# Kernel tuning notes

Hardware: AMD Instinct MI355X
Metric: run time of the kernel (lower is better)

## Reference

```python
import jax, jax.numpy as jnp
import numpy as np

D_MODEL = 1024   # 'seq_len' arg = input feature dim
FF_DIM = 1024
SCALE = 0.03125  # 1/sqrt(1024)


def setup_inputs() -> dict:
    key = jax.random.key(0)
    ks = jax.random.split(key, 7)
    B, T = 8, 2048
    s = 1.0 / np.sqrt(D_MODEL)
    return {
        "sequence": jax.random.normal(ks[0], (B, T, D_MODEL), dtype=jnp.float32),
        "Wq": jax.random.uniform(ks[1], (FF_DIM, D_MODEL), jnp.float32, -s, s),
        "bq": jax.random.uniform(ks[2], (FF_DIM,), jnp.float32, -s, s),
        "Wk": jax.random.uniform(ks[3], (FF_DIM, D_MODEL), jnp.float32, -s, s),
        "bk": jax.random.uniform(ks[4], (FF_DIM,), jnp.float32, -s, s),
        "Wv": jax.random.uniform(ks[5], (FF_DIM, D_MODEL), jnp.float32, -s, s),
        "bv": jax.random.uniform(ks[6], (FF_DIM,), jnp.float32, -s, s),
    }


def reference(sequence, Wq, bq, Wk, bk, Wv, bv):
    # Q/K/V linear projections (torch Linear: x @ W.T + b)
    q = jnp.einsum('btd,fd->btf', sequence, Wq) + bq
    k = jnp.einsum('btd,fd->btf', sequence, Wk) + bk
    v = jnp.einsum('btd,fd->btf', sequence, Wv) + bv
    # scaled dot-product attention (dropout p=0 -> identity)
    scores = jnp.einsum('btf,bsf->bts', q, k) * SCALE  # [B,T,T]
    attn = jax.nn.softmax(scores, axis=-1)
    return jnp.einsum('bts,bsf->btf', attn, v)
```

## Files before the change

### kernel.cpp

```cpp
#include <hip/hip_runtime.h>
#include <hip/hip_bf16.h>

#define BB 8
#define TT 2048
#define DD 1024
#define FF 1024

typedef __attribute__((ext_vector_type(8))) short bf16x8;
typedef __attribute__((ext_vector_type(4))) float f32x4;
typedef __attribute__((ext_vector_type(4))) short s16x4;

constexpr float kScaleLog2e = 0.03125f * 1.44269504088896340736f;

__device__ __forceinline__ short bf16_bits(float x) {
    __hip_bfloat16 h = __float2bfloat16(x);
    short s;
    __builtin_memcpy(&s, &h, sizeof(short));
    return s;
}

__global__ __launch_bounds__(256) void cvt_all(
    const float* __restrict__ seq, const float* __restrict__ Wq,
    const float* __restrict__ Wk, const float* __restrict__ Wv,
    short* __restrict__ seqb, short* __restrict__ Wb)
{
    const int bid = blockIdx.x;
    const float* src;
    short* dst;
    int i;
    if (bid < 8192)      { src = seq; dst = seqb;                      i = bid * 256 + threadIdx.x; }
    else if (bid < 8704) { src = Wq;  dst = Wb;                        i = (bid - 8192) * 256 + threadIdx.x; }
    else if (bid < 9216) { src = Wk;  dst = Wb + (size_t)FF * DD;      i = (bid - 8704) * 256 + threadIdx.x; }
    else                 { src = Wv;  dst = Wb + (size_t)2 * FF * DD;  i = (bid - 9216) * 256 + threadIdx.x; }
    f32x4 a = ((const f32x4*)src)[2 * i];
    f32x4 b = ((const f32x4*)src)[2 * i + 1];
    bf16x8 o;
#pragma unroll
    for (int j = 0; j < 4; ++j) { o[j] = bf16_bits(a[j]); o[4 + j] = bf16_bits(b[j]); }
    ((bf16x8*)dst)[i] = o;
}

#define SLOT 8192

__device__ __forceinline__ void stage2(const short* g0, const short* g1,
                                       short* slot, int lo0, int lo1) {
    __builtin_amdgcn_global_load_lds(
        (const __attribute__((address_space(1))) unsigned int*)g0,
        (__attribute__((address_space(3))) unsigned int*)(slot + lo0), 16, 0, 0);
    __builtin_amdgcn_global_load_lds(
        (const __attribute__((address_space(1))) unsigned int*)g1,
        (__attribute__((address_space(3))) unsigned int*)(slot + lo1), 16, 0, 0);
}

template<int W>
__device__ __forceinline__ void tile_barrier() {
    if constexpr (W == 8)      asm volatile("s_waitcnt vmcnt(8)" ::: "memory");
    else if constexpr (W == 4) asm volatile("s_waitcnt vmcnt(4)" ::: "memory");
    else if constexpr (W == 0) asm volatile("s_waitcnt vmcnt(0)" ::: "memory");
    __builtin_amdgcn_s_barrier();
    __builtin_amdgcn_sched_barrier(0);
}

__device__ __forceinline__ void lgkm_gate() {
    asm volatile("s_waitcnt lgkmcnt(0)" ::: "memory");
    __builtin_amdgcn_sched_barrier(0);
}

template<bool S12, bool S34, int WMID, int WEND>
__device__ __forceinline__ void tile_body(
    int t, short* As, short* Bs,
    const short* a0, const short* a1, const short* b0, const short* b1,
    int lo0, int lo1, int wm, int wn, int rk, f32x4 (&acc)[8][4])
{
    const short* sA0 = As + ((2 * t) & 3) * SLOT;
    const short* sB0 = Bs + ((2 * t) & 3) * SLOT;
    const short* sA1 = As + ((2 * t + 1) & 3) * SLOT;
    const short* sB1 = Bs + ((2 * t + 1) & 3) * SLOT;

    bf16x8 a[4], b[4];

#pragma unroll
    for (int m = 0; m < 4; ++m) a[m] = *(const bf16x8*)(sA0 + (wm + m * 16) * 32 + rk);
#pragma unroll
    for (int n = 0; n < 4; ++n) b[n] = *(const bf16x8*)(sB0 + (wn + n * 16) * 32 + rk);
    if constexpr (S12)
        stage2(a0 + (2 * t + 3) * 32, a1 + (2 * t + 3) * 32,
               As + ((2 * t + 3) & 3) * SLOT, lo0, lo1);
    lgkm_gate();
    __builtin_amdgcn_s_setprio(1);
#pragma unroll
    for (int m = 0; m < 4; ++m)
#pragma unroll
        for (int n = 0; n < 4; ++n)
            acc[m][n] = __builtin_amdgcn_mfma_f32_16x16x32_bf16(a[m], b[n], acc[m][n], 0, 0, 0);
    __builtin_amdgcn_s_setprio(0);

#pragma unroll
    for (int m = 0; m < 4; ++m) a[m] = *(const bf16x8*)(sA0 + (wm + 64 + m * 16) * 32 + rk);
    if constexpr (S12)
        stage2(b0 + (2 * t + 3) * 32, b1 + (2 * t + 3) * 32,
               Bs + ((2 * t + 3) & 3) * SLOT, lo0, lo1);
    lgkm_gate();
    __builtin_amdgcn_s_setprio(1);
#pragma unroll
    for (int m = 0; m < 4; ++m)
#pragma unroll
        for (int n = 0; n < 4; ++n)
            acc[m + 4][n] = __builtin_amdgcn_mfma_f32_16x16x32_bf16(a[m], b[n], acc[m + 4][n], 0, 0, 0);
    __builtin_amdgcn_s_setprio(0);

    tile_barrier<WMID>();

#pragma unroll
    for (int m = 0; m < 4; ++m) a[m] = *(const bf16x8*)(sA1 + (wm + m * 16) * 32 + rk);
#pragma unroll
    for (int n = 0; n < 4; ++n) b[n] = *(const bf16x8*)(sB1 + (wn + n * 16) * 32 + rk);
    if constexpr (S34)
        stage2(a0 + (2 * t + 4) * 32, a1 + (2 * t + 4) * 32,
               As + ((2 * t + 4) & 3) * SLOT, lo0, lo1);
    lgkm_gate();
    __builtin_amdgcn_s_setprio(1);
#pragma unroll
    for (int m = 0; m < 4; ++m)
#pragma unroll
        for (int n = 0; n < 4; ++n)
            acc[m][n] = __builtin_amdgcn_mfma_f32_16x16x32_bf16(a[m], b[n], acc[m][n], 0, 0, 0);
    __builtin_amdgcn_s_setprio(0);

#pragma unroll
    for (int m = 0; m < 4; ++m) a[m] = *(const bf16x8*)(sA1 + (wm + 64 + m * 16) * 32 + rk);
    if constexpr (S34)
        stage2(b0 + (2 * t + 4) * 32, b1 + (2 * t + 4) * 32,
               Bs + ((2 * t + 4) & 3) * SLOT, lo0, lo1);
    lgkm_gate();
    __builtin_amdgcn_s_setprio(1);
#pragma unroll
    for (int m = 0; m < 4; ++m)
#pragma unroll
        for (int n = 0; n < 4; ++n)
            acc[m + 4][n] = __builtin_amdgcn_mfma_f32_16x16x32_bf16(a[m], b[n], acc[m + 4][n], 0, 0, 0);
    __builtin_amdgcn_s_setprio(0);

    if constexpr (WEND >= 0)
        tile_barrier<WEND>();
}

__device__ __forceinline__ void gemm256(
    const short* __restrict__ A, int lda, int m0,
    const short* __restrict__ B, int ldb, int n0,
    int T, short* As, short* Bs, f32x4 (&acc)[8][4])
{
    const int tid  = threadIdx.x;
    const int lane = tid & 63;
    const int w    = tid >> 6;
    const int wm   = (w >> 2) * 128;
    const int wn   = (w & 3) * 64;
    const int r    = lane & 15;
    const int qd   = lane >> 4;
    const int rk   = r * 32 + (qd ^ ((r >> 1) & 3)) * 8;

    const int s0   = w * 128 + lane, s1 = s0 + 64;
    const int row0 = s0 >> 2,  row1 = s1 >> 2;
    const int cl0  = (s0 & 3) ^ ((row0 >> 1) & 3);
    const int cl1  = (s1 & 3) ^ ((row1 >> 1) & 3);
    const short* a0 = A + (size_t)(m0 + row0) * lda + cl0 * 8;
    const short* a1 = A + (size_t)(m0 + row1) * lda + cl1 * 8;
    const short* b0 = B + (size_t)(n0 + row0) * ldb + cl0 * 8;
    const short* b1 = B + (size_t)(n0 + row1) * ldb + cl1 * 8;
    const int lo0 = s0 * 8, lo1 = s1 * 8;

    stage2(a0,      a1,      As,            lo0, lo1);
    stage2(b0,      b1,      Bs,            lo0, lo1);
    stage2(a0 + 32, a1 + 32, As + SLOT,     lo0, lo1);
    stage2(b0 + 32, b1 + 32, Bs + SLOT,     lo0, lo1);
    stage2(a0 + 64, a1 + 64, As + 2 * SLOT, lo0, lo1);
    stage2(b0 + 64, b1 + 64, Bs + 2 * SLOT, lo0, lo1);
    tile_barrier<8>();

    for (int t = 0; t < T - 2; ++t)
        tile_body<true, true, 8, 8>(t, As, Bs, a0, a1, b0, b1, lo0, lo1, wm, wn, rk, acc);
    tile_body<true,  false, 8, 4>(T - 2, As, Bs, a0, a1, b0, b1, lo0, lo1, wm, wn, rk, acc);
    tile_body<false, false, 0, -1>(T - 1, As, Bs, a0, a1, b0, b1, lo0, lo1, wm, wn, rk, acc);
}

__global__ __launch_bounds__(512, 2) void qkv256(
    const short* __restrict__ seqb, const short* __restrict__ Wb,
    const float* __restrict__ bq, const float* __restrict__ bk,
    const float* __restrict__ bv,
    __hip_bfloat16* __restrict__ q, __hip_bfloat16* __restrict__ k,
    __hip_bfloat16* __restrict__ vT)
{
    __shared__ short As[4 * SLOT], Bs[4 * SLOT];
    const int bid  = blockIdx.x;
    const int id2  = (bid & 7) * 96 + (bid >> 3);
    const int mt   = id2 / 12;
    const int rest = id2 - mt * 12;
    const int nt   = rest & 3;
    const int proj = rest >> 2;

    const short* W    = Wb + (size_t)proj * FF * DD;
    const float* bias = proj == 0 ? bq : (proj == 1 ? bk : bv);

    f32x4 acc[8][4];
#pragma unroll
    for (int m = 0; m < 8; ++m)
#pragma unroll
        for (int n = 0; n < 4; ++n) acc[m][n] = (f32x4){0.f, 0.f, 0.f, 0.f};

    gemm256(seqb, DD, mt * 256, W, DD, nt * 256, DD / 64, As, Bs, acc);

    const int lane = threadIdx.x & 63;
    const int w    = threadIdx.x >> 6;
    const int wm   = (w >> 2) * 128;
    const int wn   = (w & 3) * 64;
    const int r    = lane & 15;
    const int qd   = lane >> 4;
    const int row_base = mt * 256 + wm + qd * 4;
    const int col_base = nt * 256 + wn + r;

    if (proj < 2) {
        __hip_bfloat16* dst = (proj == 0) ? q : k;
#pragma unroll
        for (int nf = 0; nf < 4; ++nf) {
            const int col = col_base + nf * 16;
            const float bv_ = bias[col];
#pragma unroll
            for (int mf = 0; mf < 8; ++mf)
#pragma unroll
                for (int i = 0; i < 4; ++i)
                    dst[(size_t)(row_base + mf * 16 + i) * FF + col] =
                        __float2bfloat16(acc[mf][nf][i] + bv_);
        }
    } else {
#pragma unroll
        for (int mf = 0; mf < 8; ++mf) {
            const int rowg = row_base + mf * 16;
            const int b_   = rowg >> 11;
            const int t_   = rowg & 2047;
            __hip_bfloat16* vb = vT + (size_t)b_ * FF * TT;
#pragma unroll
            for (int nf = 0; nf < 4; ++nf) {
                const int col = col_base + nf * 16;
                const float bvv = bias[col];
                s16x4 pack;
#pragma unroll
                for (int i = 0; i < 4; ++i) pack[i] = bf16_bits(acc[mf][nf][i] + bvv);
                *(s16x4*)(vb + (size_t)col * TT + t_) = pack;
            }
        }
    }
}

__global__ __launch_bounds__(512, 2) void score256(
    const __hip_bfloat16* __restrict__ q, const __hip_bfloat16* __restrict__ k,
    __hip_bfloat16* __restrict__ P, float* __restrict__ Z)
{
    __shared__ short As[4 * SLOT], Bs[4 * SLOT];
    const int bid = blockIdx.x;
    const int id2 = (bid & 7) * 64 + (bid >> 3);
    const int b   = id2 >> 6;
    const int tt  = (id2 >> 3) & 7;
    const int st  = id2 & 7;

    const short* qb = (const short*)q + (size_t)b * TT * FF;
    const short* kb = (const short*)k + (size_t)b * TT * FF;

    f32x4 acc[8][4];
#pragma unroll
    for (int m = 0; m < 8; ++m)
#pragma unroll
        for (int n = 0; n < 4; ++n) acc[m][n] = (f32x4){0.f, 0.f, 0.f, 0.f};

    gemm256(qb, FF, tt * 256, kb, FF, st * 256, FF / 64, As, Bs, acc);

    const int lane = threadIdx.x & 63;
    const int w    = threadIdx.x >> 6;
    const int wm   = (w >> 2) * 128;
    const int wn   = (w & 3) * 64;
    const int r    = lane & 15;
    const int qd   = lane >> 4;
    const int row_base = tt * 256 + wm + qd * 4;
    const int col_base = st * 256 + wn + r;

    __hip_bfloat16* Pb = P + (size_t)b * TT * TT;
    float* Zb = Z + b * TT;

    float rs[8][4];
#pragma unroll
    for (int mf = 0; mf < 8; ++mf)
#pragma unroll
        for (int i = 0; i < 4; ++i) rs[mf][i] = 0.f;

#pragma unroll
    for (int mf = 0; mf < 8; ++mf)
#pragma unroll
        for (int nf = 0; nf < 4; ++nf) {
            const int col = col_base + nf * 16;
#pragma unroll
            for (int i = 0; i < 4; ++i) {
                const float e = exp2f(acc[mf][nf][i] * kScaleLog2e);
                const __hip_bfloat16 eb = __float2bfloat16(e);
                rs[mf][i] += __bfloat162float(eb);
                Pb[(size_t)(row_base + mf * 16 + i) * TT + col] = eb;
            }
        }
#pragma unroll
    for (int off = 1; off < 16; off <<= 1)
#pragma unroll
        for (int mf = 0; mf < 8; ++mf)
#pragma unroll
            for (int i = 0; i < 4; ++i) rs[mf][i] += __shfl_xor(rs[mf][i], off, 64);
    if (r == 0) {
#pragma unroll
        for (int mf = 0; mf < 8; ++mf)
#pragma unroll
            for (int i = 0; i < 4; ++i)
                atomicAdd(&Zb[row_base + mf * 16 + i], rs[mf][i]);
    }
}

__global__ __launch_bounds__(512, 2) void pv256(
    const __hip_bfloat16* __restrict__ P, const __hip_bfloat16* __restrict__ vT,
    const float* __restrict__ Z, float* __restrict__ out)
{
    __shared__ short As[4 * SLOT], Bs[4 * SLOT];
    const int bid = blockIdx.x;
    const int id2 = (bid & 7) * 32 + (bid >> 3);
    const int b   = id2 >> 5;
    const int tt  = (id2 >> 2) & 7;
    const int ft  = id2 & 3;

    const short* Pb = (const short*)P + (size_t)b * TT * TT;
    const short* vb = (const short*)vT + (size_t)b * FF * TT;

    f32x4 acc[8][4];
#pragma unroll
    for (int m = 0; m < 8; ++m)
#pragma unroll
        for (int n = 0; n < 4; ++n) acc[m][n] = (f32x4){0.f, 0.f, 0.f, 0.f};

    gemm256(Pb, TT, tt * 256, vb, TT, ft * 256, TT / 64, As, Bs, acc);

    const int lane = threadIdx.x & 63;
    const int w    = threadIdx.x >> 6;
    const int wm   = (w >> 2) * 128;
    const int wn   = (w & 3) * 64;
    const int r    = lane & 15;
    const int qd   = lane >> 4;
    const int row_base = tt * 256 + wm + qd * 4;
    const int col_base = ft * 256 + wn + r;

    const float* Zb = Z + b * TT;
    float* ob = out + (size_t)b * TT * FF;

#pragma unroll
    for (int mf = 0; mf < 8; ++mf) {
        float rz[4];
#pragma unroll
        for (int i = 0; i < 4; ++i) rz[i] = 1.0f / Zb[row_base + mf * 16 + i];
#pragma unroll
        for (int nf = 0; nf < 4; ++nf) {
            const int col = col_base + nf * 16;
#pragma unroll
            for (int i = 0; i < 4; ++i)
                ob[(size_t)(row_base + mf * 16 + i) * FF + col] = acc[mf][nf][i] * rz[i];
        }
    }
}

extern "C" void kernel_launch(void* const* d_in, const int* in_sizes, int n_in,
                              void* d_out, int out_size, void* d_ws, size_t ws_size,
                              hipStream_t stream) {
    const float* seq = (const float*)d_in[0];
    const float* Wq  = (const float*)d_in[1];
    const float* bq  = (const float*)d_in[2];
    const float* Wk  = (const float*)d_in[3];
    const float* bk  = (const float*)d_in[4];
    const float* Wv  = (const float*)d_in[5];
    const float* bv  = (const float*)d_in[6];
    float* out = (float*)d_out;
    char* ws = (char*)d_ws;

    const size_t MB32 = 33554432;
    __hip_bfloat16* q   = (__hip_bfloat16*)(ws);
    __hip_bfloat16* k   = (__hip_bfloat16*)(ws + MB32);
    __hip_bfloat16* vT  = (__hip_bfloat16*)(ws + 2 * MB32);
    __hip_bfloat16* P   = (__hip_bfloat16*)(ws + 3 * MB32);
    float*          Z   = (float*)(ws + 3 * MB32 + (size_t)67108864);
    short*          seqb = (short*)P;
    short*          Wb   = (short*)((char*)P + MB32);

    hipMemsetAsync(Z, 0, (size_t)BB * TT * sizeof(float), stream);

    cvt_all<<<9728, 256, 0, stream>>>(seq, Wq, Wk, Wv, seqb, Wb);
    qkv256<<<768, 512, 0, stream>>>(seqb, Wb, bq, bk, bv, q, k, vT);
    score256<<<BB * 64, 512, 0, stream>>>(q, k, P, Z);
    pv256<<<BB * 32, 512, 0, stream>>>(P, vT, Z, out);
}
```

Baseline: 408.4 us.

## Software-pipeline LDS fragment loads ahead of MFMAs in QKV GEMM main loop

Restructures the QKV projection GEMM inner loop so LDS fragment reads for the next sub-tile are issued before the current MFMA block runs, and the first fragments of the next tile are prefetched into registers carried across iterations. Full lgkmcnt(0) gates are replaced by partial lgkmcnt waits, and there is now one vmcnt barrier per half-tile instead of two per tile. The aim is to hide LDS latency behind MFMA work, at the cost of more live registers (extra fragment arrays), which risks spills under launch_bounds(512,2).

```diff
diff --git a/kernel.cpp b/kernel.cpp
--- a/kernel.cpp
+++ b/kernel.cpp
@@ -52,97 +52,102 @@
         (__attribute__((address_space(3))) unsigned int*)(slot + lo1), 16, 0, 0);
 }
 
-template<int W>
-__device__ __forceinline__ void tile_barrier() {
-    if constexpr (W == 8)      asm volatile("s_waitcnt vmcnt(8)" ::: "memory");
-    else if constexpr (W == 4) asm volatile("s_waitcnt vmcnt(4)" ::: "memory");
-    else if constexpr (W == 0) asm volatile("s_waitcnt vmcnt(0)" ::: "memory");
-    __builtin_amdgcn_s_barrier();
-    __builtin_amdgcn_sched_barrier(0);
-}
-
-__device__ __forceinline__ void lgkm_gate() {
-    asm volatile("s_waitcnt lgkmcnt(0)" ::: "memory");
-    __builtin_amdgcn_sched_barrier(0);
-}
-
-template<bool S12, bool S34, int WMID, int WEND>
+__device__ __forceinline__ void sbar() { __builtin_amdgcn_sched_barrier(0); }
+
+template<int N>
+__device__ __forceinline__ void lgkm() {
+    if constexpr (N == 12)     asm volatile("s_waitcnt lgkmcnt(12)" ::: "memory");
+    else if constexpr (N == 8) asm volatile("s_waitcnt lgkmcnt(8)"  ::: "memory");
+    else if constexpr (N == 4) asm volatile("s_waitcnt lgkmcnt(4)"  ::: "memory");
+    else                       asm volatile("s_waitcnt lgkmcnt(0)"  ::: "memory");
+}
+
+__device__ __forceinline__ void mfma16(const bf16x8 (&a)[4], const bf16x8 (&b)[4],
+                                       f32x4 (&acc)[8][4], int mo) {
+#pragma unroll
+    for (int m = 0; m < 4; ++m)
+#pragma unroll
+        for (int n = 0; n < 4; ++n)
+            acc[m + mo][n] = __builtin_amdgcn_mfma_f32_16x16x32_bf16(a[m], b[n], acc[m + mo][n], 0, 0, 0);
+}
+
+template<int MODE>
 __device__ __forceinline__ void tile_body(
     int t, short* As, short* Bs,
-    const short* a0, const short* a1, const short* b0, const short* b1,
-    int lo0, int lo1, int wm, int wn, int rk, f32x4 (&acc)[8][4])
+    const short* a0g, const short* a1g, const short* b0g, const short* b1g,
+    int lo0, int lo1, int wm, int wn, int rk,
+    f32x4 (&acc)[8][4], bf16x8 (&ra)[4], bf16x8 (&rb)[4])
 {
     const short* sA0 = As + ((2 * t) & 3) * SLOT;
-    const short* sB0 = Bs + ((2 * t) & 3) * SLOT;
     const short* sA1 = As + ((2 * t + 1) & 3) * SLOT;
     const short* sB1 = Bs + ((2 * t + 1) & 3) * SLOT;
 
-    bf16x8 a[4], b[4];
-
-#pragma unroll
-    for (int m = 0; m < 4; ++m) a[m] = *(const bf16x8*)(sA0 + (wm + m * 16) * 32 + rk);
-#pragma unroll
-    for (int n = 0; n < 4; ++n) b[n] = *(const bf16x8*)(sB0 + (wn + n * 16) * 32 + rk);
-    if constexpr (S12)
-        stage2(a0 + (2 * t + 3) * 32, a1 + (2 * t + 3) * 32,
+    bf16x8 a2[4], a3[4], b3[4], a4[4];
+
+#pragma unroll
+    for (int m = 0; m < 4; ++m) a2[m] = *(const bf16x8*)(sA0 + (wm + 64 + m * 16) * 32 + rk);
+#pragma unroll
+    for (int m = 0; m < 4; ++m) a3[m] = *(const bf16x8*)(sA1 + (wm + m * 16) * 32 + rk);
+#pragma unroll
+    for (int n = 0; n < 4; ++n) b3[n] = *(const bf16x8*)(sB1 + (wn + n * 16) * 32 + rk);
+    if constexpr (MODE <= 1) {
+        stage2(a0g + (2 * t + 3) * 32, a1g + (2 * t + 3) * 32,
                As + ((2 * t + 3) & 3) * SLOT, lo0, lo1);
-    lgkm_gate();
+        stage2(b0g + (2 * t + 3) * 32, b1g + (2 * t + 3) * 32,
+               Bs + ((2 * t + 3) & 3) * SLOT, lo0, lo1);
+    }
+    sbar(); lgkm<12>(); sbar();
     __builtin_amdgcn_s_setprio(1);
-#pragma unroll
-    for (int m = 0; m < 4; ++m)
-#pragma unroll
-        for (int n = 0; n < 4; ++n)
-            acc[m][n] = __builtin_amdgcn_mfma_f32_16x16x32_bf16(a[m], b[n], acc[m][n], 0, 0, 0);
+    mfma16(ra, rb, acc, 0);
     __builtin_amdgcn_s_setprio(0);
 
 #pragma unroll
-    for (int m = 0; m < 4; ++m) a[m] = *(const bf16x8*)(sA0 + (wm + 64 + m * 16) * 32 + rk);
-    if constexpr (S12)
-        stage2(b0 + (2 * t + 3) * 32, b1 + (2 * t + 3) * 32,
-               Bs + ((2 * t + 3) & 3) * SLOT, lo0, lo1);
-    lgkm_gate();
+    for (int m = 0; m < 4; ++m) a4[m] = *(const bf16x8*)(sA1 + (wm + 64 + m * 16) * 32 + rk);
+    sbar(); lgkm<12>(); sbar();
     __builtin_amdgcn_s_setprio(1);
-#pragma unroll
-    for (int m = 0; m < 4; ++m)
-#pragma unroll
-        for (int n = 0; n < 4; ++n)
-            acc[m + 4][n] = __builtin_amdgcn_mfma_f32_16x16x32_bf16(a[m], b[n], acc[m + 4][n], 0, 0, 0);
+    mfma16(a2, rb, acc, 4);
     __builtin_amdgcn_s_setprio(0);
 
-    tile_barrier<WMID>();
-
-#pragma unroll
-    for (int m = 0; m < 4; ++m) a[m] = *(const bf16x8*)(sA1 + (wm + m * 16) * 32 + rk);
-#pragma unroll
-    for (int n = 0; n < 4; ++n) b[n] = *(const bf16x8*)(sB1 + (wn + n * 16) * 32 + rk);
-    if constexpr (S34)
-        stage2(a0 + (2 * t + 4) * 32, a1 + (2 * t + 4) * 32,
+    if constexpr (MODE <= 1) {
+        asm volatile("s_waitcnt vmcnt(4)" ::: "memory");
+        __builtin_amdgcn_s_barrier();
+        sbar();
+    }
+    if constexpr (MODE == 0) {
+        stage2(a0g + (2 * t + 4) * 32, a1g + (2 * t + 4) * 32,
                As + ((2 * t + 4) & 3) * SLOT, lo0, lo1);
-    lgkm_gate();
+        stage2(b0g + (2 * t + 4) * 32, b1g + (2 * t + 4) * 32,
+               Bs + ((2 * t + 4) & 3) * SLOT, lo0, lo1);
+    }
+    sbar(); lgkm<4>(); sbar();
     __builtin_amdgcn_s_setprio(1);
-#pragma unroll
-    for (int m = 0; m < 4; ++m)
-#pragma unroll
-        for (int n = 0; n < 4; ++n)
-            acc[m][n] = __builtin_amdgcn_mfma_f32_16x16x32_bf16(a[m], b[n], acc[m][n], 0, 0, 0);
+    mfma16(a3, b3, acc, 0);
     __builtin_amdgcn_s_setprio(0);
 
-#pragma unroll
-    for (int m = 0; m < 4; ++m) a[m] = *(const bf16x8*)(sA1 + (wm + 64 + m * 16) * 32 + rk);
-    if constexpr (S34)
-        stage2(b0 + (2 * t + 4) * 32, b1 + (2 * t + 4) * 32,
-               Bs + ((2 * t + 4) & 3) * SLOT, lo0, lo1);
-    lgkm_gate();
+    if constexpr (MODE <= 1) {
+        const short* sAn = As + ((2 * t + 2) & 3) * SLOT;
+        const short* sBn = Bs + ((2 * t + 2) & 3) * SLOT;
+#pragma unroll
+        for (int m = 0; m < 4; ++m) ra[m] = *(const bf16x8*)(sAn + (wm + m * 16) * 32 + rk);
+#pragma unroll
+        for (int n = 0; n < 4; ++n) rb[n] = *(const bf16x8*)(sBn + (wn + n * 16) * 32 + rk);
+    }
+    sbar();
+    if constexpr (MODE <= 1) { lgkm<8>(); } else { lgkm<0>(); }
+    sbar();
     __builtin_amdgcn_s_setprio(1);
-#pragma unroll
-    for (int m = 0; m < 4; ++m)
-#pragma unroll
-        for (int n = 0; n < 4; ++n)
-            acc[m + 4][n] = __builtin_amdgcn_mfma_f32_16x16x32_bf16(a[m], b[n], acc[m + 4][n], 0, 0, 0);
+    mfma16(a4, b3, acc, 4);
     __builtin_amdgcn_s_setprio(0);
 
-    if constexpr (WEND >= 0)
-        tile_barrier<WEND>();
+    if constexpr (MODE == 0) {
+        asm volatile("s_waitcnt vmcnt(4)" ::: "memory");
+        __builtin_amdgcn_s_barrier();
+        sbar();
+    } else if constexpr (MODE == 1) {
+        asm volatile("s_waitcnt vmcnt(0)" ::: "memory");
+        __builtin_amdgcn_s_barrier();
+        sbar();
+    }
 }
 
 __device__ __forceinline__ void gemm256(
@@ -175,12 +180,20 @@
     stage2(b0 + 32, b1 + 32, Bs + SLOT,     lo0, lo1);
     stage2(a0 + 64, a1 + 64, As + 2 * SLOT, lo0, lo1);
     stage2(b0 + 64, b1 + 64, Bs + 2 * SLOT, lo0, lo1);
-    tile_barrier<8>();
+    asm volatile("s_waitcnt vmcnt(4)" ::: "memory");
+    __builtin_amdgcn_s_barrier();
+    sbar();
+
+    bf16x8 ra[4], rb[4];
+#pragma unroll
+    for (int m = 0; m < 4; ++m) ra[m] = *(const bf16x8*)(As + (wm + m * 16) * 32 + rk);
+#pragma unroll
+    for (int n = 0; n < 4; ++n) rb[n] = *(const bf16x8*)(Bs + (wn + n * 16) * 32 + rk);
 
     for (int t = 0; t < T - 2; ++t)
-        tile_body<true, true, 8, 8>(t, As, Bs, a0, a1, b0, b1, lo0, lo1, wm, wn, rk, acc);
-    tile_body<true,  false, 8, 4>(T - 2, As, Bs, a0, a1, b0, b1, lo0, lo1, wm, wn, rk, acc);
-    tile_body<false, false, 0, -1>(T - 1, As, Bs, a0, a1, b0, b1, lo0, lo1, wm, wn, rk, acc);
+        tile_body<0>(t, As, Bs, a0, a1, b0, b1, lo0, lo1, wm, wn, rk, acc, ra, rb);
+    tile_body<1>(T - 2, As, Bs, a0, a1, b0, b1, lo0, lo1, wm, wn, rk, acc, ra, rb);
+    tile_body<2>(T - 1, As, Bs, a0, a1, b0, b1, lo0, lo1, wm, wn, rk, acc, ra, rb);
 }
 
 __global__ __launch_bounds__(512, 2) void qkv256(
```

New measurement: 410.8 us. About the same (+0.6%).

## Fold Wq and Wk into a combined matrix to drop the K projection

Applied to the files above, without the earlier changes.

Rewrites the scores as X·(Wq^T Wk)·X^T plus a per-key bias term, with terms that are constant along each softmax row dropped. A small GEMM forms W2 = Wq^T·Wk once per call and projects X with it in place of computing Q and K separately. The score GEMM then reads the bf16 X directly as keys. This removes one of the three large projection GEMMs and the K write, at the cost of a split-K weight GEMM, a reduction kernel, an extra bf16 rounding of the combined weights, and the key bias folded into the conversion pass via a dot product.

```diff
diff --git a/kernel.cpp b/kernel.cpp
--- a/kernel.cpp
+++ b/kernel.cpp
@@ -19,25 +19,92 @@
     return s;
 }
 
+__global__ __launch_bounds__(256) void wv2k(
+    const float* __restrict__ Wk, const float* __restrict__ bq,
+    float* __restrict__ wv2)
+{
+    const int d = blockIdx.x * 256 + threadIdx.x;
+    float acc = 0.f;
+#pragma unroll 8
+    for (int f = 0; f < 1024; ++f) acc += Wk[(size_t)f * 1024 + d] * bq[f];
+    wv2[d] = acc;
+}
+
 __global__ __launch_bounds__(256) void cvt_all(
     const float* __restrict__ seq, const float* __restrict__ Wq,
     const float* __restrict__ Wk, const float* __restrict__ Wv,
-    short* __restrict__ seqb, short* __restrict__ Wb)
-{
+    const float* __restrict__ wv2,
+    short* __restrict__ Xbuf, short* __restrict__ Wvb,
+    short* __restrict__ WqT, short* __restrict__ WkT,
+    float* __restrict__ w)
+{
+    __shared__ float red[256];
+    __shared__ short ldt[64 * 66];
     const int bid = blockIdx.x;
-    const float* src;
-    short* dst;
-    int i;
-    if (bid < 8192)      { src = seq; dst = seqb;                      i = bid * 256 + threadIdx.x; }
-    else if (bid < 8704) { src = Wq;  dst = Wb;                        i = (bid - 8192) * 256 + threadIdx.x; }
-    else if (bid < 9216) { src = Wk;  dst = Wb + (size_t)FF * DD;      i = (bid - 8704) * 256 + threadIdx.x; }
-    else                 { src = Wv;  dst = Wb + (size_t)2 * FF * DD;  i = (bid - 9216) * 256 + threadIdx.x; }
-    f32x4 a = ((const f32x4*)src)[2 * i];
-    f32x4 b = ((const f32x4*)src)[2 * i + 1];
-    bf16x8 o;
-#pragma unroll
-    for (int j = 0; j < 4; ++j) { o[j] = bf16_bits(a[j]); o[4 + j] = bf16_bits(b[j]); }
-    ((bf16x8*)dst)[i] = o;
+    const int tid = threadIdx.x;
+
+    if (bid < 8192) {
+        const int i = bid * 256 + tid;
+        f32x4 a = ((const f32x4*)seq)[2 * i];
+        f32x4 b = ((const f32x4*)seq)[2 * i + 1];
+        bf16x8 o;
+        const int col0 = (tid & 127) * 8;
+        float part = 0.f;
+#pragma unroll
+        for (int j = 0; j < 4; ++j) {
+            o[j] = bf16_bits(a[j]);     part += a[j] * wv2[col0 + j];
+            o[4 + j] = bf16_bits(b[j]); part += b[j] * wv2[col0 + 4 + j];
+        }
+        ((bf16x8*)Xbuf)[i] = o;
+        red[tid] = part;
+        __syncthreads();
+#pragma unroll
+        for (int s = 64; s >= 1; s >>= 1) {
+            if ((tid & 127) < s) red[tid] += red[tid + s];
+            __syncthreads();
+        }
+        if (tid == 0)   w[bid * 2]     = red[0];
+        if (tid == 128) w[bid * 2 + 1] = red[128];
+        return;
+    }
+    if (bid < 8704) {
+        const int i = (bid - 8192) * 256 + tid;
+        f32x4 a = ((const f32x4*)Wv)[2 * i];
+        f32x4 b = ((const f32x4*)Wv)[2 * i + 1];
+        bf16x8 o;
+#pragma unroll
+        for (int j = 0; j < 4; ++j) { o[j] = bf16_bits(a[j]); o[4 + j] = bf16_bits(b[j]); }
+        ((bf16x8*)Wvb)[i] = o;
+        return;
+    }
+    const float* src = (bid < 8960) ? Wq : Wk;
+    short* dst       = (bid < 8960) ? WqT : WkT;
+    const int tt = (bid < 8960) ? (bid - 8704) : (bid - 8960);
+    const int tr = tt >> 4, tc = tt & 15;
+    {
+        const int fr = tid >> 2, dg = tid & 3;
+        const float* s0 = src + (size_t)(tr * 64 + fr) * 1024 + tc * 64 + dg * 16;
+#pragma unroll
+        for (int q = 0; q < 4; ++q) {
+            f32x4 a = ((const f32x4*)s0)[q];
+#pragma unroll
+            for (int j = 0; j < 4; ++j)
+                ldt[(dg * 16 + q * 4 + j) * 66 + fr] = bf16_bits(a[j]);
+        }
+    }
+    __syncthreads();
+    {
+        const int dr = tid >> 2, fg = tid & 3;
+        bf16x8 o0, o1;
+#pragma unroll
+        for (int j = 0; j < 8; ++j) {
+            o0[j] = ldt[dr * 66 + fg * 16 + j];
+            o1[j] = ldt[dr * 66 + fg * 16 + 8 + j];
+        }
+        short* d0 = dst + (size_t)(tc * 64 + dr) * 1024 + tr * 64 + fg * 16;
+        *(bf16x8*)d0 = o0;
+        *(bf16x8*)(d0 + 8) = o1;
+    }
 }
 
 #define SLOT 8192
@@ -183,23 +250,72 @@
     tile_body<false, false, 0, -1>(T - 1, As, Bs, a0, a1, b0, b1, lo0, lo1, wm, wn, rk, acc);
 }
 
-__global__ __launch_bounds__(512, 2) void qkv256(
-    const short* __restrict__ seqb, const short* __restrict__ Wb,
-    const float* __restrict__ bq, const float* __restrict__ bk,
-    const float* __restrict__ bv,
-    __hip_bfloat16* __restrict__ q, __hip_bfloat16* __restrict__ k,
-    __hip_bfloat16* __restrict__ vT)
+__global__ __launch_bounds__(512, 2) void w2split(
+    const short* __restrict__ WkT, const short* __restrict__ WqT,
+    float* __restrict__ Wpart)
+{
+    __shared__ short As[4 * SLOT], Bs[4 * SLOT];
+    const int gt = blockIdx.x >> 3, slice = blockIdx.x & 7;
+    const int gm = gt >> 2, gn = gt & 3;
+
+    f32x4 acc[8][4];
+#pragma unroll
+    for (int m = 0; m < 8; ++m)
+#pragma unroll
+        for (int n = 0; n < 4; ++n) acc[m][n] = (f32x4){0.f, 0.f, 0.f, 0.f};
+
+    gemm256(WkT + slice * 128, 1024, gm * 256,
+            WqT + slice * 128, 1024, gn * 256, 2, As, Bs, acc);
+
+    const int lane = threadIdx.x & 63;
+    const int w    = threadIdx.x >> 6;
+    const int wm   = (w >> 2) * 128;
+    const int wn   = (w & 3) * 64;
+    const int r    = lane & 15;
+    const int qd   = lane >> 4;
+    const int row_base = gm * 256 + wm + qd * 4;
+    const int col_base = gn * 256 + wn + r;
+    float* dst = Wpart + (size_t)slice * 1048576;
+#pragma unroll
+    for (int mf = 0; mf < 8; ++mf)
+#pragma unroll
+        for (int nf = 0; nf < 4; ++nf)
+#pragma unroll
+            for (int i = 0; i < 4; ++i)
+                dst[(size_t)(row_base + mf * 16 + i) * 1024 + col_base + nf * 16] = acc[mf][nf][i];
+}
+
+__global__ __launch_bounds__(256) void w2red(
+    const float* __restrict__ Wpart, short* __restrict__ W2Tb)
+{
+    const int base = blockIdx.x * 1024 + threadIdx.x * 4;
+    f32x4 s = (f32x4){0.f, 0.f, 0.f, 0.f};
+#pragma unroll
+    for (int sl = 0; sl < 8; ++sl) {
+        f32x4 p = *(const f32x4*)(Wpart + (size_t)sl * 1048576 + base);
+#pragma unroll
+        for (int j = 0; j < 4; ++j) s[j] += p[j];
+    }
+    s16x4 o;
+#pragma unroll
+    for (int j = 0; j < 4; ++j) o[j] = bf16_bits(s[j]);
+    *(s16x4*)(W2Tb + base) = o;
+}
+
+__global__ __launch_bounds__(512, 2) void proj(
+    const short* __restrict__ Xbuf, const short* __restrict__ W2Tb,
+    const short* __restrict__ Wvb, const float* __restrict__ bv,
+    __hip_bfloat16* __restrict__ Ybuf, __hip_bfloat16* __restrict__ vT)
 {
     __shared__ short As[4 * SLOT], Bs[4 * SLOT];
     const int bid  = blockIdx.x;
-    const int id2  = (bid & 7) * 96 + (bid >> 3);
-    const int mt   = id2 / 12;
-    const int rest = id2 - mt * 12;
+    const int id2  = (bid & 7) * 64 + (bid >> 3);
+    const int mt   = id2 >> 3;
+    const int rest = id2 & 7;
     const int nt   = rest & 3;
-    const int proj = rest >> 2;
-
-    const short* W    = Wb + (size_t)proj * FF * DD;
-    const float* bias = proj == 0 ? bq : (proj == 1 ? bk : bv);
+    const int p    = rest >> 2;
+
+    const short* W = (p == 0) ? W2Tb : Wvb;
 
     f32x4 acc[8][4];
 #pragma unroll
@@ -207,7 +323,7 @@
 #pragma unroll
         for (int n = 0; n < 4; ++n) acc[m][n] = (f32x4){0.f, 0.f, 0.f, 0.f};
 
-    gemm256(seqb, DD, mt * 256, W, DD, nt * 256, DD / 64, As, Bs, acc);
+    gemm256(Xbuf, DD, mt * 256, W, DD, nt * 256, DD / 64, As, Bs, acc);
 
     const int lane = threadIdx.x & 63;
     const int w    = threadIdx.x >> 6;
@@ -218,18 +334,16 @@
     const int row_base = mt * 256 + wm + qd * 4;
     const int col_base = nt * 256 + wn + r;
 
-    if (proj < 2) {
-        __hip_bfloat16* dst = (proj == 0) ? q : k;
+    if (p == 0) {
 #pragma unroll
         for (int nf = 0; nf < 4; ++nf) {
             const int col = col_base + nf * 16;
-            const float bv_ = bias[col];
 #pragma unroll
             for (int mf = 0; mf < 8; ++mf)
 #pragma unroll
                 for (int i = 0; i < 4; ++i)
-                    dst[(size_t)(row_base + mf * 16 + i) * FF + col] =
-                        __float2bfloat16(acc[mf][nf][i] + bv_);
+                    Ybuf[(size_t)(row_base + mf * 16 + i) * FF + col] =
+                        __float2bfloat16(acc[mf][nf][i]);
         }
     } else {
 #pragma unroll
@@ -241,7 +355,7 @@
 #pragma unroll
             for (int nf = 0; nf < 4; ++nf) {
                 const int col = col_base + nf * 16;
-                const float bvv = bias[col];
+                const float bvv = bv[col];
                 s16x4 pack;
 #pragma unroll
                 for (int i = 0; i < 4; ++i) pack[i] = bf16_bits(acc[mf][nf][i] + bvv);
@@ -252,8 +366,9 @@
 }
 
 __global__ __launch_bounds__(512, 2) void score256(
-    const __hip_bfloat16* __restrict__ q, const __hip_bfloat16* __restrict__ k,
-    __hip_bfloat16* __restrict__ P, float* __restrict__ Z)
+    const __hip_bfloat16* __restrict__ Ybuf, const short* __restrict__ Xbuf,
+    const float* __restrict__ w, __hip_bfloat16* __restrict__ P,
+    float* __restrict__ Z)
 {
     __shared__ short As[4 * SLOT], Bs[4 * SLOT];
     const int bid = blockIdx.x;
@@ -262,8 +377,8 @@
     const int tt  = (id2 >> 3) & 7;
     const int st  = id2 & 7;
 
-    const short* qb = (const short*)q + (size_t)b * TT * FF;
-    const short* kb = (const short*)k + (size_t)b * TT * FF;
+    const short* yb = (const short*)Ybuf + (size_t)b * TT * FF;
+    const short* xb = Xbuf + (size_t)b * TT * FF;
 
     f32x4 acc[8][4];
 #pragma unroll
@@ -271,12 +386,12 @@
 #pragma unroll
         for (int n = 0; n < 4; ++n) acc[m][n] = (f32x4){0.f, 0.f, 0.f, 0.f};
 
-    gemm256(qb, FF, tt * 256, kb, FF, st * 256, FF / 64, As, Bs, acc);
+    gemm256(yb, FF, tt * 256, xb, FF, st * 256, FF / 64, As, Bs, acc);
 
     const int lane = threadIdx.x & 63;
-    const int w    = threadIdx.x >> 6;
-    const int wm   = (w >> 2) * 128;
-    const int wn   = (w & 3) * 64;
+    const int wv   = threadIdx.x >> 6;
+    const int wm   = (wv >> 2) * 128;
+    const int wn   = (wv & 3) * 64;
     const int r    = lane & 15;
     const int qd   = lane >> 4;
     const int row_base = tt * 256 + wm + qd * 4;
@@ -284,6 +399,7 @@
 
     __hip_bfloat16* Pb = P + (size_t)b * TT * TT;
     float* Zb = Z + b * TT;
+    const float* wb = w + (size_t)b * TT;
 
     float rs[8][4];
 #pragma unroll
@@ -292,18 +408,19 @@
         for (int i = 0; i < 4; ++i) rs[mf][i] = 0.f;
 
 #pragma unroll
-    for (int mf = 0; mf < 8; ++mf)
-#pragma unroll
-        for (int nf = 0; nf < 4; ++nf) {
-            const int col = col_base + nf * 16;
+    for (int nf = 0; nf < 4; ++nf) {
+        const int col = col_base + nf * 16;
+        const float ws_ = wb[col];
+#pragma unroll
+        for (int mf = 0; mf < 8; ++mf)
 #pragma unroll
             for (int i = 0; i < 4; ++i) {
-                const float e = exp2f(acc[mf][nf][i] * kScaleLog2e);
+                const float e = exp2f((acc[mf][nf][i] + ws_) * kScaleLog2e);
                 const __hip_bfloat16 eb = __float2bfloat16(e);
                 rs[mf][i] += __bfloat162float(eb);
                 Pb[(size_t)(row_base + mf * 16 + i) * TT + col] = eb;
             }
-        }
+    }
 #pragma unroll
     for (int off = 1; off < 16; off <<= 1)
 #pragma unroll
@@ -375,25 +492,33 @@
     const float* Wq  = (const float*)d_in[1];
     const float* bq  = (const float*)d_in[2];
     const float* Wk  = (const float*)d_in[3];
-    const float* bk  = (const float*)d_in[4];
+    const float* bk  = (const float*)d_in[4];  (void)bk;
     const float* Wv  = (const float*)d_in[5];
     const float* bv  = (const float*)d_in[6];
     float* out = (float*)d_out;
     char* ws = (char*)d_ws;
 
     const size_t MB32 = 33554432;
-    __hip_bfloat16* q   = (__hip_bfloat16*)(ws);
-    __hip_bfloat16* k   = (__hip_bfloat16*)(ws + MB32);
-    __hip_bfloat16* vT  = (__hip_bfloat16*)(ws + 2 * MB32);
-    __hip_bfloat16* P   = (__hip_bfloat16*)(ws + 3 * MB32);
-    float*          Z   = (float*)(ws + 3 * MB32 + (size_t)67108864);
-    short*          seqb = (short*)P;
-    short*          Wb   = (short*)((char*)P + MB32);
-
+    short* Xbuf = (short*)(ws);
+    __hip_bfloat16* Ybuf = (__hip_bfloat16*)(ws + MB32);
+    __hip_bfloat16* vT   = (__hip_bfloat16*)(ws + 2 * MB32);
+    char*  Pr   = ws + 3 * MB32;
+    __hip_bfloat16* P = (__hip_bfloat16*)Pr;
+    short* WqT  = (short*)(Pr);
+    short* WkT  = (short*)(Pr + 2097152);
+    short* Wvb  = (short*)(Pr + 4194304);
+    short* W2Tb = (short*)(Pr + 6291456);
+    float* Wpart= (float*)(Pr + 8388608);
+    float* Z    = (float*)(ws + 3 * MB32 + (size_t)67108864);
+    float* wv2  = Z;
+    float* w    = (float*)d_out;
+
+    wv2k<<<4, 256, 0, stream>>>(Wk, bq, wv2);
+    cvt_all<<<9216, 256, 0, stream>>>(seq, Wq, Wk, Wv, wv2, Xbuf, Wvb, WqT, WkT, w);
+    w2split<<<128, 512, 0, stream>>>(WkT, WqT, Wpart);
+    w2red<<<1024, 256, 0, stream>>>(Wpart, W2Tb);
+    proj<<<512, 512, 0, stream>>>(Xbuf, W2Tb, Wvb, bv, Ybuf, vT);
     hipMemsetAsync(Z, 0, (size_t)BB * TT * sizeof(float), stream);
-
-    cvt_all<<<9728, 256, 0, stream>>>(seq, Wq, Wk, Wv, seqb, Wb);
-    qkv256<<<768, 512, 0, stream>>>(seqb, Wb, bq, bk, bv, q, k, vT);
-    score256<<<BB * 64, 512, 0, stream>>>(q, k, P, Z);
+    score256<<<BB * 64, 512, 0, stream>>>(Ybuf, Xbuf, w, P, Z);
     pv256<<<BB * 32, 512, 0, stream>>>(P, vT, Z, out);
 }
```

Measured after the change: 472.8 us. 1.16x slower.
